# Optimization experiments

Measured on AMD Instinct MI355X. Metric: run time of the kernel, lower is better.

Reference implementation:

```python
import jax, jax.numpy as jnp
import numpy as np

B, N, D_FEAT = 16, 4096, 64
NPOINT, NSAMPLE = 1024, 32
MLP = [64, 64, 128]
IN_CH = 3 + D_FEAT
EPS = 1e-5  # BatchNorm eps (torch default)


def _fps(xyz, npoint):
    # Farthest point sampling; sequential scan over npoint steps (matches torch loop).
    b, n, _ = xyz.shape
    def step(carry, _):
        distance, farthest = carry  # (B,N) running min dist, (B,) current centroid idx
        centroid = jnp.take_along_axis(xyz, farthest[:, None, None], axis=1)  # (B,1,3)
        d = jnp.sum((xyz - centroid) ** 2, -1)  # (B,N)
        distance = jnp.minimum(distance, d)
        nxt = jnp.argmax(distance, -1).astype(jnp.int32)
        return (distance, nxt), farthest
    init = (jnp.full((b, n), jnp.inf, dtype=xyz.dtype),
            jnp.full((b,), n // 2, dtype=jnp.int32))
    _, centroids = jax.lax.scan(step, init, None, length=npoint)
    return centroids.T  # (B, npoint)


def _gather(pts, idx):
    # pts: (B,N,C); idx: (B,...) int -> (B,...,C)
    return jax.vmap(lambda p, i: p[i])(pts, idx)


def setup_inputs() -> dict:
    key = jax.random.key(0)
    ks = jax.random.split(key, 16)
    inp = {
        'xyz': jax.random.normal(ks[0], (B, N, 3), jnp.float32),
        'points': jax.random.normal(ks[1], (B, N, D_FEAT), jnp.float32),
    }
    last = IN_CH
    for li, oc in enumerate(MLP):
        inp[f'W{li}'] = jax.random.normal(ks[2 + li], (oc, last), jnp.float32) * (1.0 / np.sqrt(last))
        inp[f'b{li}'] = jnp.zeros((oc,), jnp.float32)
        inp[f'g{li}'] = jnp.ones((oc,), jnp.float32)
        inp[f'be{li}'] = jnp.zeros((oc,), jnp.float32)
        last = oc
    C = MLP[-1]; R = C // 8
    inp['aW1'] = jax.random.normal(ks[10], (R, C), jnp.float32) * (1.0 / np.sqrt(C))
    inp['aW2'] = jax.random.normal(ks[11], (C, R), jnp.float32) * (1.0 / np.sqrt(R))
    return inp


def reference(xyz, points, W0, b0, g0, be0, W1, b1, g1, be1, W2, b2, g2, be2, aW1, aW2):
    fps_idx = _fps(xyz, NPOINT)                 # (B,S) int32
    new_xyz = _gather(xyz, fps_idx)             # (B,S,3)
    # squared distances (B,S,N) via matmul expansion (as torch square_distance)
    d = (-2.0 * jnp.einsum('bsc,bnc->bsn', new_xyz, xyz)
         + jnp.sum(new_xyz ** 2, -1)[..., None]
         + jnp.sum(xyz ** 2, -1)[:, None, :])
    _, idx = jax.lax.top_k(-d, NSAMPLE)         # (B,S,k) nearest neighbors
    grouped_xyz = _gather(xyz, idx)             # (B,S,k,3)
    rel = grouped_xyz - new_xyz[:, :, None, :]  # relative coords
    feat = _gather(points, idx)                 # (B,S,k,D)
    g = jnp.concatenate([rel, feat], axis=-1)   # (B,S,k,3+D) channels-last
    # 1x1 conv MLP + BatchNorm (training-mode batch stats) + ReLU
    for (W, b, ga, be) in ((W0, b0, g0, be0), (W1, b1, g1, be1), (W2, b2, g2, be2)):
        g = jnp.einsum('bskc,oc->bsko', g, W) + b
        mu = g.mean(axis=(0, 1, 2))
        var = g.var(axis=(0, 1, 2))
        g = ga * (g - mu) * jax.lax.rsqrt(var + EPS) + be
        g = jax.nn.relu(g)
    new_points = g.max(axis=2)                  # max over nsample -> (B,S,C)
    # channel attention on (B,C,S) == reductions over S here
    avg = new_points.mean(axis=1)               # (B,C)
    mx = new_points.max(axis=1)                 # (B,C)
    def fc(v):
        return jnp.einsum('cr,br->bc', aW2, jax.nn.relu(jnp.einsum('rc,bc->br', aW1, v)))
    scale = jax.nn.sigmoid(fc(avg) + fc(mx))    # (B,C)
    new_points = new_points * scale[:, None, :]
    return new_xyz, new_points, fps_idx
```

## Files before the change

### kernel.cpp

```cpp
#include <hip/hip_runtime.h>
#include <hip/hip_bf16.h>

#define BB 16
#define NN 4096
#define SS 1024
#define KS 32
#define DF 64
#define INC 67
#define C1 64
#define C2 64
#define C3 128
#define ROWS (BB*SS*KS)
#define EPSBN 1e-5f
#define F_INF (__builtin_inff())

typedef __bf16 bf16;
typedef __bf16 bfrag __attribute__((ext_vector_type(8)));
typedef float  ffrag __attribute__((ext_vector_type(4)));
typedef float  f2    __attribute__((ext_vector_type(2)));
typedef unsigned long long u64;

#define OUT_NXYZ 0
#define OUT_NP   49152
#define OUT_FPS  2146304

#define OFF_FPS   0u
#define OFF_NXYZ  65536u
#define OFF_IDX   262144u
#define OFF_STATS 2359296u
#define OFF_ASUM  2555904u
#define OFF_AMAX  2621440u
#define OFF_BNC   2686976u
#define OFF_SCALE 2690048u
#define OFF_NP0   2698240u
#define OFF_YMAX  11086848u
#define OFF_H1    19475456u
#define OFF_H2    86584320u
#define ZERO_BYTES (196608u + 65536u + 65536u)

#define DPP_MAX_STEP(k, ctrl, rmask, bc) { \
  int _lo = __builtin_amdgcn_update_dpp(0, (int)(unsigned)(k), (ctrl), (rmask), 0xf, (bc)); \
  int _hi = __builtin_amdgcn_update_dpp(0, (int)((k)>>32),     (ctrl), (rmask), 0xf, (bc)); \
  u64 _k2 = ((u64)(unsigned)_hi << 32) | (unsigned)_lo; \
  if (_k2 > (k)) (k) = _k2; }

#define DPP_FMAX_STEP(v, ctrl, rmask, bc) { \
  int _t = __builtin_amdgcn_update_dpp(0, __float_as_int(v), (ctrl), (rmask), 0xf, (bc)); \
  (v) = fmaxf((v), __uint_as_float((unsigned)_t)); }

__device__ __forceinline__ u64 dpp_wavemax64(u64 k){
  DPP_MAX_STEP(k, 0x111, 0xf, true)
  DPP_MAX_STEP(k, 0x112, 0xf, true)
  DPP_MAX_STEP(k, 0x114, 0xf, true)
  DPP_MAX_STEP(k, 0x118, 0xf, true)
  DPP_MAX_STEP(k, 0x142, 0xa, false)
  DPP_MAX_STEP(k, 0x143, 0xc, false)
  return k;
}

__device__ __forceinline__ u64 readlane64(u64 k, int lane){
  unsigned lo = (unsigned)__builtin_amdgcn_readlane((int)(unsigned)k, lane);
  unsigned hi = (unsigned)__builtin_amdgcn_readlane((int)(k >> 32),   lane);
  return ((u64)hi << 32) | lo;
}

__device__ __forceinline__ u64 umax64(u64 a, u64 b){ return a > b ? a : b; }

__global__ __launch_bounds__(256) void fps_kernel(const float* __restrict__ xyz,
                                                  int* __restrict__ fps_i,
                                                  float* __restrict__ nxyz_ws,
                                                  float* __restrict__ out)
{
  #pragma clang fp contract(off)
  __shared__ __align__(16) float4 lc[NN];
  __shared__ int lfps[SS];
  __shared__ __align__(16) u64 slotk[2][4];
  int b = blockIdx.x, t = threadIdx.x;
  const float* xb = xyz + (size_t)b*NN*3;
  for (int p = t; p < NN; p += 256){
    lc[p] = make_float4(xb[p*3], xb[p*3+1], xb[p*3+2], 0.f);
  }
  __syncthreads();
  f2 px2[8], py2[8], pz2[8], pd2[8];
  int p0 = t*16;
  #pragma unroll
  for (int j=0;j<8;++j){
    float4 a = lc[p0+2*j], c = lc[p0+2*j+1];
    px2[j] = (f2){a.x, c.x}; py2[j] = (f2){a.y, c.y}; pz2[j] = (f2){a.z, c.z};
    pd2[j] = (f2){F_INF, F_INF};
  }
  float cx = lc[NN/2].x, cy = lc[NN/2].y, cz = lc[NN/2].z;
  if (t==0) lfps[0]=NN/2;
  int wv = t >> 6, lane = t & 63;
  for (int it=1; it<SS; ++it){
    f2 c2x = (f2){cx,cx}, c2y = (f2){cy,cy}, c2z = (f2){cz,cz};
    float bv=-1.f; int bi=p0;
    #pragma unroll
    for (int j=0;j<8;++j){
      f2 dx = px2[j]-c2x, dy = py2[j]-c2y, dz = pz2[j]-c2z;
      f2 d = (dx*dx + dy*dy) + dz*dz;
      f2 nd = (f2){fminf(pd2[j].x, d.x), fminf(pd2[j].y, d.y)};
      pd2[j]=nd;
      if (nd.x > bv){ bv=nd.x; bi=p0+2*j; }
      if (nd.y > bv){ bv=nd.y; bi=p0+2*j+1; }
    }
    float mv = bv;
    DPP_FMAX_STEP(mv, 0x111, 0xf, true)
    DPP_FMAX_STEP(mv, 0x112, 0xf, true)
    DPP_FMAX_STEP(mv, 0x114, 0xf, true)
    DPP_FMAX_STEP(mv, 0x118, 0xf, true)
    DPP_FMAX_STEP(mv, 0x142, 0xa, false)
    DPP_FMAX_STEP(mv, 0x143, 0xc, false)
    float wmax = __uint_as_float((unsigned)__builtin_amdgcn_readlane(__float_as_int(mv), 63));
    u64 em = __ballot(bv == wmax);
    int wl = (int)__builtin_ctzll(em);
    int wbi = __builtin_amdgcn_readlane(bi, wl);
    int p = it & 1;
    if (lane == 0)
      slotk[p][wv] = ((u64)__float_as_uint(wmax) << 32) | (unsigned)(~wbi);
    __syncthreads();
    ulonglong2 sA = *(const ulonglong2*)&slotk[p][0];
    ulonglong2 sB = *(const ulonglong2*)&slotk[p][2];
    u64 k = umax64(umax64(sA.x, sA.y), umax64(sB.x, sB.y));
    int i = ~(unsigned)k;
    float4 cc = lc[i];
    cx = cc.x; cy = cc.y; cz = cc.z;
    if (t==0) lfps[it]=i;
  }
  __syncthreads();
  for (int s=t; s<SS; s+=256){
    int i = lfps[s];
    fps_i[b*SS+s]=i;
    out[OUT_FPS + b*SS + s] = (float)i;
    float4 cc = lc[i];
    int o3 = (b*SS+s)*3;
    out[OUT_NXYZ+o3]=cc.x; out[OUT_NXYZ+o3+1]=cc.y; out[OUT_NXYZ+o3+2]=cc.z;
    nxyz_ws[o3]=cc.x; nxyz_ws[o3+1]=cc.y; nxyz_ws[o3+2]=cc.z;
  }
}

__global__ __launch_bounds__(64) void knn_kernel(const float* __restrict__ xyz,
                                                 const float* __restrict__ nxyz,
                                                 int* __restrict__ knn)
{
  __shared__ float ld[NN];
  int lane = threadIdx.x;
  int bs = blockIdx.x;
  int b = bs >> 10;
  const float* xb = xyz + (size_t)b*NN*3;
  float sx=nxyz[bs*3], sy=nxyz[bs*3+1], sz=nxyz[bs*3+2];
  float gv[8]; int gi[8];
  float lv = F_INF; int li = 0;
  #pragma unroll
  for (int g=0; g<8; ++g){
    float bgv = F_INF; int bgi = 0;
    #pragma unroll
    for (int jj=0; jj<8; ++jj){
      int p = (g*8+jj)*64 + lane;
      float dx=xb[p*3]-sx, dy=xb[p*3+1]-sy, dz=xb[p*3+2]-sz;
      float d = dx*dx+dy*dy+dz*dz;
      ld[p] = d;
      if (d < bgv){ bgv=d; bgi=p; }
    }
    gv[g]=bgv; gi[g]=bgi;
    if (bgv < lv){ lv=bgv; li=bgi; }
  }
  int kept = 0;
  for (int it=0; it<KS; ++it){
    u64 mk = ~(((u64)__float_as_uint(lv) << 32) | (unsigned)li);
    mk = dpp_wavemax64(mk);
    mk = readlane64(mk, 63);
    int i = (int)(unsigned)(~mk);
    if (lane==it) kept = i;
    if ((i & 63) == lane){
      int j = i >> 6;
      ld[i] = F_INF;
      int g = j >> 3;
      float bgv=F_INF; int bgi=0;
      for (int jj=0;jj<8;++jj){
        int p = (g*8+jj)*64 + lane;
        float d = ld[p];
        if (d<bgv){bgv=d;bgi=p;}
      }
      #pragma unroll
      for (int q=0;q<8;++q){ if (q==g){ gv[q]=bgv; gi[q]=bgi; } }
      lv=F_INF; li=0;
      #pragma unroll
      for (int q=0;q<8;++q){ if (gv[q]<lv){ lv=gv[q]; li=gi[q]; } }
    }
  }
  if (lane < KS) knn[bs*KS + lane] = kept;
}

__global__ __launch_bounds__(512) void conv1_kernel(const float* __restrict__ xyz,
                                                    const float* __restrict__ points,
                                                    const float* __restrict__ W0,
                                                    const float* __restrict__ b0,
                                                    const float* __restrict__ nxyz,
                                                    const int* __restrict__ knn,
                                                    bf16* __restrict__ h1,
                                                    float* __restrict__ stats)
{
  __shared__ __align__(16) bf16 As[128][104];
  __shared__ __align__(16) bf16 Bs[64][104];
  __shared__ float s1[C1], s2[C1];
  int t = threadIdx.x;
  int Rbase = blockIdx.x * 128;
  if (t < C1){ s1[t]=0.f; s2[t]=0.f; }
  if (t < 256){
    int o = t >> 2, q = t & 3;
    const float* wr = W0 + o*INC;
    for (int cc = q*24; cc < q*24+24; ++cc){
      float w;
      if (cc < 64) w = wr[3+cc];
      else if (cc < 67) w = wr[cc-64];
      else w = 0.f;
      Bs[o][cc] = (bf16)w;
    }
  }
  {
    int r = t >> 2, q = t & 3;
    int R = Rbase + r;
    int bs = R >> 5;
    int bIdx = bs >> 10;
    int nI = knn[R];
    const float* pr = points + ((size_t)(bIdx*NN + nI))*DF + q*16;
    float4 f0 = *(const float4*)(pr);
    float4 f1 = *(const float4*)(pr+4);
    float4 f2v = *(const float4*)(pr+8);
    float4 f3 = *(const float4*)(pr+12);
    bf16* ap = &As[r][q*16];
    ap[0]=(bf16)f0.x; ap[1]=(bf16)f0.y; ap[2]=(bf16)f0.z; ap[3]=(bf16)f0.w;
    ap[4]=(bf16)f1.x; ap[5]=(bf16)f1.y; ap[6]=(bf16)f1.z; ap[7]=(bf16)f1.w;
    ap[8]=(bf16)f2v.x; ap[9]=(bf16)f2v.y; ap[10]=(bf16)f2v.z; ap[11]=(bf16)f2v.w;
    ap[12]=(bf16)f3.x; ap[13]=(bf16)f3.y; ap[14]=(bf16)f3.z; ap[15]=(bf16)f3.w;
    if (q==0){
      const float* xr = xyz + ((size_t)(bIdx*NN + nI))*3;
      const float* nr = nxyz + bs*3;
      As[r][64]=(bf16)(xr[0]-nr[0]);
      As[r][65]=(bf16)(xr[1]-nr[1]);
      As[r][66]=(bf16)(xr[2]-nr[2]);
      for (int cc=67; cc<96; ++cc) As[r][cc]=(bf16)0.f;
    }
  }
  __syncthreads();
  int wv = t >> 6, lane = t & 63;
  int row16 = wv * 16;
  int arow = lane & 15, kgrp = lane >> 4;
  ffrag acc[4] = {};
  #pragma unroll
  for (int kc = 0; kc < 3; ++kc){
    bfrag af = *(const bfrag*)&As[row16 + arow][kc*32 + kgrp*8];
    #pragma unroll
    for (int nt = 0; nt < 4; ++nt){
      bfrag bfv = *(const bfrag*)&Bs[nt*16 + arow][kc*32 + kgrp*8];
      acc[nt] = __builtin_amdgcn_mfma_f32_16x16x32_bf16(af, bfv, acc[nt], 0,0,0);
    }
  }
  #pragma unroll
  for (int nt=0; nt<4; ++nt){
    int c = nt*16 + arow;
    float bias = b0[c];
    float ls1=0.f, ls2=0.f;
    #pragma unroll
    for (int r=0;r<4;++r){
      float y = acc[nt][r] + bias;
      int grow = Rbase + row16 + kgrp*4 + r;
      h1[(size_t)grow*C1 + c] = (bf16)y;
      ls1 += y; ls2 += y*y;
    }
    ls1 += __shfl_xor(ls1, 16); ls1 += __shfl_xor(ls1, 32);
    ls2 += __shfl_xor(ls2, 16); ls2 += __shfl_xor(ls2, 32);
    if (kgrp==0){ atomicAdd(&s1[c], ls1); atomicAdd(&s2[c], ls2); }
  }
  __syncthreads();
  if (t < C1){
    float* gp = stats + (blockIdx.x & 63)*256;
    atomicAdd(&gp[t], s1[t]);
    atomicAdd(&gp[128 + t], s2[t]);
  }
}

__global__ __launch_bounds__(512) void conv2_kernel(const bf16* __restrict__ h1,
                                                    const float* __restrict__ W1,
                                                    const float* __restrict__ b1,
                                                    const float* __restrict__ stats0,
                                                    const float* __restrict__ g0,
                                                    const float* __restrict__ be0,
                                                    bf16* __restrict__ h2,
                                                    float* __restrict__ stats)
{
  __shared__ __align__(16) bf16 As[128][72];
  __shared__ __align__(16) bf16 Bs[64][72];
  __shared__ float s1[C2], s2[C2];
  __shared__ float sbA[C2], sbB[C2];
  int t = threadIdx.x;
  int Rbase = blockIdx.x * 128;
  if (t < C2){ s1[t]=0.f; s2[t]=0.f; }
  if (t < C2){
    float a1=0.f, a2=0.f;
    for (int q=0;q<64;++q){ a1 += stats0[q*256+t]; a2 += stats0[q*256+128+t]; }
    float inv = 1.f/(float)ROWS;
    float mu = a1*inv; float var = a2*inv - mu*mu;
    float a = g0[t]*rsqrtf(var + EPSBN);
    sbA[t] = a; sbB[t] = be0[t] - mu*a;
  }
  if (t < 256){
    int o = t >> 2, q = t & 3;
    const float* wr = W1 + o*64 + q*16;
    bf16* bp = &Bs[o][q*16];
    #pragma unroll
    for (int v=0; v<4; ++v){
      float4 f = *(const float4*)(wr + v*4);
      bp[v*4+0]=(bf16)f.x; bp[v*4+1]=(bf16)f.y; bp[v*4+2]=(bf16)f.z; bp[v*4+3]=(bf16)f.w;
    }
  }
  __syncthreads();
  {
    int r = t >> 2, q = t & 3;
    int R = Rbase + r;
    const bf16* hr = h1 + (size_t)R*64 + q*16;
    bfrag h0 = *(const bfrag*)hr;
    bfrag h1v = *(const bfrag*)(hr+8);
    #pragma unroll
    for (int j=0;j<8;++j){
      int c=q*16+j;
      As[r][c] = (bf16)fmaxf(fmaf(sbA[c], (float)h0[j], sbB[c]), 0.f);
    }
    #pragma unroll
    for (int j=0;j<8;++j){
      int c=q*16+8+j;
      As[r][c] = (bf16)fmaxf(fmaf(sbA[c], (float)h1v[j], sbB[c]), 0.f);
    }
  }
  __syncthreads();
  int wv = t >> 6, lane = t & 63;
  int row16 = wv * 16;
  int arow = lane & 15, kgrp = lane >> 4;
  ffrag acc[4] = {};
  #pragma unroll
  for (int kc = 0; kc < 2; ++kc){
    bfrag af = *(const bfrag*)&As[row16 + arow][kc*32 + kgrp*8];
    #pragma unroll
    for (int nt = 0; nt < 4; ++nt){
      bfrag bfv = *(const bfrag*)&Bs[nt*16 + arow][kc*32 + kgrp*8];
      acc[nt] = __builtin_amdgcn_mfma_f32_16x16x32_bf16(af, bfv, acc[nt], 0,0,0);
    }
  }
  #pragma unroll
  for (int nt=0; nt<4; ++nt){
    int c = nt*16 + arow;
    float bias = b1[c];
    float ls1=0.f, ls2=0.f;
    #pragma unroll
    for (int r=0;r<4;++r){
      float y = acc[nt][r] + bias;
      int grow = Rbase + row16 + kgrp*4 + r;
      h2[(size_t)grow*C2 + c] = (bf16)y;
      ls1 += y; ls2 += y*y;
    }
    ls1 += __shfl_xor(ls1, 16); ls1 += __shfl_xor(ls1, 32);
    ls2 += __shfl_xor(ls2, 16); ls2 += __shfl_xor(ls2, 32);
    if (kgrp==0){ atomicAdd(&s1[c], ls1); atomicAdd(&s2[c], ls2); }
  }
  __syncthreads();
  if (t < C2){
    float* gp = stats + (blockIdx.x & 63)*256;
    atomicAdd(&gp[t], s1[t]);
    atomicAdd(&gp[128 + t], s2[t]);
  }
}

__global__ __launch_bounds__(512) void conv3_kernel(const bf16* __restrict__ h2,
                                                    const float* __restrict__ W2,
                                                    const float* __restrict__ b2,
                                                    const float* __restrict__ stats1,
                                                    const float* __restrict__ g1,
                                                    const float* __restrict__ be1,
                                                    float* __restrict__ ymax,
                                                    float* __restrict__ stats)
{
  __shared__ __align__(16) bf16 As[128][72];
  __shared__ __align__(16) bf16 Bs[128][72];
  __shared__ float s1[C3], s2[C3];
  __shared__ float wmax[8][C3];
  __shared__ float sbA[C2], sbB[C2];
  int t = threadIdx.x;
  int Rbase = blockIdx.x * 128;
  if (t < C3){ s1[t]=0.f; s2[t]=0.f; }
  if (t < C2){
    float a1=0.f, a2=0.f;
    for (int q=0;q<64;++q){ a1 += stats1[q*256+t]; a2 += stats1[q*256+128+t]; }
    float inv = 1.f/(float)ROWS;
    float mu = a1*inv; float var = a2*inv - mu*mu;
    float a = g1[t]*rsqrtf(var + EPSBN);
    sbA[t] = a; sbB[t] = be1[t] - mu*a;
  }
  if (t < 256){
    int o = t >> 1, q = t & 1;
    const float* wr = W2 + o*64 + q*32;
    bf16* bp = &Bs[o][q*32];
    #pragma unroll
    for (int v=0; v<8; ++v){
      float4 f = *(const float4*)(wr + v*4);
      bp[v*4+0]=(bf16)f.x; bp[v*4+1]=(bf16)f.y; bp[v*4+2]=(bf16)f.z; bp[v*4+3]=(bf16)f.w;
    }
  }
  __syncthreads();
  {
    int r = t >> 2, q = t & 3;
    int R = Rbase + r;
    const bf16* hr = h2 + (size_t)R*64 + q*16;
    bfrag h0 = *(const bfrag*)hr;
    bfrag h1v = *(const bfrag*)(hr+8);
    #pragma unroll
    for (int j=0;j<8;++j){
      int c=q*16+j;
      As[r][c] = (bf16)fmaxf(fmaf(sbA[c], (float)h0[j], sbB[c]), 0.f);
    }
    #pragma unroll
    for (int j=0;j<8;++j){
      int c=q*16+8+j;
      As[r][c] = (bf16)fmaxf(fmaf(sbA[c], (float)h1v[j], sbB[c]), 0.f);
    }
  }
  __syncthreads();
  int wv = t >> 6, lane = t & 63;
  int row16 = wv * 16;
  int arow = lane & 15, kgrp = lane >> 4;
  ffrag acc[8] = {};
  #pragma unroll
  for (int kc = 0; kc < 2; ++kc){
    bfrag af = *(const bfrag*)&As[row16 + arow][kc*32 + kgrp*8];
    #pragma unroll
    for (int nt = 0; nt < 8; ++nt){
      bfrag bfv = *(const bfrag*)&Bs[nt*16 + arow][kc*32 + kgrp*8];
      acc[nt] = __builtin_amdgcn_mfma_f32_16x16x32_bf16(af, bfv, acc[nt], 0,0,0);
    }
  }
  #pragma unroll
  for (int nt=0; nt<8; ++nt){
    int c = nt*16 + arow;
    float bias = b2[c];
    float ls1=0.f, ls2=0.f, mm=-F_INF;
    #pragma unroll
    for (int r=0;r<4;++r){
      float y = acc[nt][r] + bias;
      ls1 += y; ls2 += y*y; mm = fmaxf(mm, y);
    }
    ls1 += __shfl_xor(ls1, 16); ls1 += __shfl_xor(ls1, 32);
    ls2 += __shfl_xor(ls2, 16); ls2 += __shfl_xor(ls2, 32);
    mm = fmaxf(mm, __shfl_xor(mm, 16)); mm = fmaxf(mm, __shfl_xor(mm, 32));
    if (kgrp==0){ atomicAdd(&s1[c], ls1); atomicAdd(&s2[c], ls2); wmax[wv][c]=mm; }
  }
  __syncthreads();
  {
    int grp = t >> 7;
    int c = t & 127;
    float m = fmaxf(wmax[grp*2][c], wmax[grp*2+1][c]);
    ymax[(size_t)(blockIdx.x*4 + grp)*C3 + c] = m;
  }
  if (t < C3){
    float* gp = stats + (blockIdx.x & 63)*256;
    atomicAdd(&gp[t], s1[t]);
    atomicAdd(&gp[128 + t], s2[t]);
  }
}

__global__ __launch_bounds__(256) void attreduce_kernel(const float* __restrict__ ymax,
                                                        const float* __restrict__ stats2,
                                                        const float* __restrict__ g2,
                                                        const float* __restrict__ be2,
                                                        float* __restrict__ np0,
                                                        float* __restrict__ asum,
                                                        unsigned* __restrict__ amax)
{
  __shared__ float rs[256], rm[256];
  __shared__ float sbA[C3], sbB[C3];
  int t = threadIdx.x;
  if (t < C3){
    float a1=0.f, a2=0.f;
    for (int q=0;q<64;++q){ a1 += stats2[q*256+t]; a2 += stats2[q*256+128+t]; }
    float inv = 1.f/(float)ROWS;
    float mu = a1*inv; float var = a2*inv - mu*mu;
    float a = g2[t]*rsqrtf(var + EPSBN);
    sbA[t] = a; sbB[t] = be2[t] - mu*a;
  }
  __syncthreads();
  int b = blockIdx.x >> 3, sg = blockIdx.x & 7;
  int c = t & 127, h = t >> 7;
  float a = sbA[c], bb = sbB[c];
  size_t base = ((size_t)(b*1024 + sg*128 + h*64))*128 + c;
  float s = 0.f, m = 0.f;
  #pragma unroll 4
  for (int j=0;j<64;++j){
    float v = fmaxf(fmaf(a, ymax[base + (size_t)j*128], bb), 0.f);
    np0[base + (size_t)j*128] = v;
    s += v; m = fmaxf(m, v);
  }
  rs[t]=s; rm[t]=m;
  __syncthreads();
  if (t < 128){
    float s2 = rs[t] + rs[t+128];
    float m2 = fmaxf(rm[t], rm[t+128]);
    atomicAdd(&asum[b*128+t], s2);
    atomicMax(&amax[b*128+t], __float_as_uint(m2));
  }
}

__global__ __launch_bounds__(256) void attn_kernel(const float* __restrict__ asum,
                                                   const unsigned* __restrict__ amax,
                                                   const float* __restrict__ aW1,
                                                   const float* __restrict__ aW2,
                                                   float* __restrict__ scale)
{
  __shared__ float avg[16][128], mx[16][128], hA[16][16], hM[16][16];
  int t = threadIdx.x;
  for (int i=t; i<2048; i+=256){
    int b=i>>7, c=i&127;
    avg[b][c]=asum[i]*(1.f/1024.f); mx[b][c]=__uint_as_float(amax[i]);
  }
  __syncthreads();
  {
    int b=t>>4, r=t&15;
    float sa=0.f, sm=0.f;
    for (int c=0;c<128;++c){ float w=aW1[r*128+c]; sa+=w*avg[b][c]; sm+=w*mx[b][c]; }
    hA[b][r]=fmaxf(sa,0.f); hM[b][r]=fmaxf(sm,0.f);
  }
  __syncthreads();
  for (int i=t;i<2048;i+=256){
    int b=i>>7,c=i&127;
    float o=0.f;
    for (int r=0;r<16;++r){ o += aW2[c*16+r]*(hA[b][r]+hM[b][r]); }
    scale[i] = 1.f/(1.f+expf(-o));
  }
}

__global__ __launch_bounds__(256) void finout_kernel(const float* __restrict__ np0,
                                                     const float* __restrict__ scale,
                                                     float* __restrict__ out)
{
  int i = blockIdx.x*256 + threadIdx.x;
  int c = i & 127; int b = i >> 17;
  out[OUT_NP + i] = np0[i] * scale[b*128+c];
}

extern "C" void kernel_launch(void* const* d_in, const int* in_sizes, int n_in,
                              void* d_out, int out_size, void* d_ws, size_t ws_size,
                              hipStream_t stream)
{
  const float* xyz    = (const float*)d_in[0];
  const float* points = (const float*)d_in[1];
  const float* W0 = (const float*)d_in[2];
  const float* b0 = (const float*)d_in[3];
  const float* g0 = (const float*)d_in[4];
  const float* be0= (const float*)d_in[5];
  const float* W1 = (const float*)d_in[6];
  const float* b1 = (const float*)d_in[7];
  const float* g1 = (const float*)d_in[8];
  const float* be1= (const float*)d_in[9];
  const float* W2 = (const float*)d_in[10];
  const float* b2 = (const float*)d_in[11];
  const float* g2 = (const float*)d_in[12];
  const float* be2= (const float*)d_in[13];
  const float* aW1= (const float*)d_in[14];
  const float* aW2= (const float*)d_in[15];
  float* out = (float*)d_out;
  char* ws = (char*)d_ws;

  int*      fpsI  = (int*)(ws + OFF_FPS);
  float*    nxyz  = (float*)(ws + OFF_NXYZ);
  int*      knnI  = (int*)(ws + OFF_IDX);
  float*    stats = (float*)(ws + OFF_STATS);
  float*    asum  = (float*)(ws + OFF_ASUM);
  unsigned* amax  = (unsigned*)(ws + OFF_AMAX);
  float*    scl   = (float*)(ws + OFF_SCALE);
  float*    np0   = (float*)(ws + OFF_NP0);
  float*    ymax  = (float*)(ws + OFF_YMAX);
  bf16*     h1    = (bf16*)(ws + OFF_H1);
  bf16*     h2    = (bf16*)(ws + OFF_H2);

  hipMemsetAsync(ws + OFF_STATS, 0, ZERO_BYTES, stream);
  fps_kernel<<<BB, 256, 0, stream>>>(xyz, fpsI, nxyz, out);
  knn_kernel<<<BB*SS, 64, 0, stream>>>(xyz, nxyz, knnI);
  conv1_kernel<<<ROWS/128, 512, 0, stream>>>(xyz, points, W0, b0, nxyz, knnI, h1, stats);
  conv2_kernel<<<ROWS/128, 512, 0, stream>>>(h1, W1, b1, stats, g0, be0, h2, stats + 64*256);
  conv3_kernel<<<ROWS/128, 512, 0, stream>>>(h2, W2, b2, stats + 64*256, g1, be1, ymax, stats + 2*64*256);
  attreduce_kernel<<<BB*8, 256, 0, stream>>>(ymax, stats + 2*64*256, g2, be2, np0, asum, amax);
  attn_kernel<<<1, 256, 0, stream>>>(asum, amax, aW1, aW2, scl);
  finout_kernel<<<(BB*SS*C3)/256, 256, 0, stream>>>(np0, scl, out);
}
```

Measured before the change: 1.024 ms.

## Pad xyz to float4 for kNN, drop np0 buffer, widen attreduce grid

FPS now also writes a float4-padded copy of xyz to the workspace, so kNN can do one vector load per point instead of three strided scalar loads. The attreduce kernel no longer writes the normalized np0 tensor. It stores the BN scale and shift so finout can recompute the BN+ReLU from ymax, which removes an 8 MB write and read. The attreduce grid is widened from 128 to 512 blocks to add parallelism. The cost is an extra 1 MB write in FPS and more atomics in attreduce.

```diff
diff --git a/kernel.cpp b/kernel.cpp
--- a/kernel.cpp
+++ b/kernel.cpp
@@ -32,7 +32,7 @@
 #define OFF_AMAX  2621440u
 #define OFF_BNC   2686976u
 #define OFF_SCALE 2690048u
-#define OFF_NP0   2698240u
+#define OFF_XYZ4  2698240u
 #define OFF_YMAX  11086848u
 #define OFF_H1    19475456u
 #define OFF_H2    86584320u
@@ -69,6 +69,7 @@
 __global__ __launch_bounds__(256) void fps_kernel(const float* __restrict__ xyz,
                                                   int* __restrict__ fps_i,
                                                   float* __restrict__ nxyz_ws,
+                                                  float4* __restrict__ xyz4,
                                                   float* __restrict__ out)
 {
   #pragma clang fp contract(off)
@@ -81,6 +82,7 @@
     lc[p] = make_float4(xb[p*3], xb[p*3+1], xb[p*3+2], 0.f);
   }
   __syncthreads();
+  for (int p = t; p < NN; p += 256) xyz4[(size_t)b*NN + p] = lc[p];
   f2 px2[8], py2[8], pz2[8], pd2[8];
   int p0 = t*16;
   #pragma unroll
@@ -139,7 +141,7 @@
   }
 }
 
-__global__ __launch_bounds__(64) void knn_kernel(const float* __restrict__ xyz,
+__global__ __launch_bounds__(64) void knn_kernel(const float4* __restrict__ xyz4,
                                                  const float* __restrict__ nxyz,
                                                  int* __restrict__ knn)
 {
@@ -147,7 +149,7 @@
   int lane = threadIdx.x;
   int bs = blockIdx.x;
   int b = bs >> 10;
-  const float* xb = xyz + (size_t)b*NN*3;
+  const float4* xb4 = xyz4 + (size_t)b*NN;
   float sx=nxyz[bs*3], sy=nxyz[bs*3+1], sz=nxyz[bs*3+2];
   float gv[8]; int gi[8];
   float lv = F_INF; int li = 0;
@@ -157,7 +159,8 @@
     #pragma unroll
     for (int jj=0; jj<8; ++jj){
       int p = (g*8+jj)*64 + lane;
-      float dx=xb[p*3]-sx, dy=xb[p*3+1]-sy, dz=xb[p*3+2]-sz;
+      float4 P = xb4[p];
+      float dx=P.x-sx, dy=P.y-sy, dz=P.z-sz;
       float d = dx*dx+dy*dy+dz*dz;
       ld[p] = d;
       if (d < bgv){ bgv=d; bgi=p; }
@@ -471,7 +474,7 @@
                                                         const float* __restrict__ stats2,
                                                         const float* __restrict__ g2,
                                                         const float* __restrict__ be2,
-                                                        float* __restrict__ np0,
+                                                        float* __restrict__ bnc,
                                                         float* __restrict__ asum,
                                                         unsigned* __restrict__ amax)
 {
@@ -485,17 +488,17 @@
     float mu = a1*inv; float var = a2*inv - mu*mu;
     float a = g2[t]*rsqrtf(var + EPSBN);
     sbA[t] = a; sbB[t] = be2[t] - mu*a;
-  }
-  __syncthreads();
-  int b = blockIdx.x >> 3, sg = blockIdx.x & 7;
+    if (blockIdx.x == 0){ bnc[t] = a; bnc[128+t] = sbB[t]; }
+  }
+  __syncthreads();
+  int b = blockIdx.x >> 5, sg = blockIdx.x & 31;
   int c = t & 127, h = t >> 7;
   float a = sbA[c], bb = sbB[c];
-  size_t base = ((size_t)(b*1024 + sg*128 + h*64))*128 + c;
+  size_t base = ((size_t)(b*1024 + sg*32 + h*16))*128 + c;
   float s = 0.f, m = 0.f;
   #pragma unroll 4
-  for (int j=0;j<64;++j){
+  for (int j=0;j<16;++j){
     float v = fmaxf(fmaf(a, ymax[base + (size_t)j*128], bb), 0.f);
-    np0[base + (size_t)j*128] = v;
     s += v; m = fmaxf(m, v);
   }
   rs[t]=s; rm[t]=m;
@@ -536,13 +539,15 @@
   }
 }
 
-__global__ __launch_bounds__(256) void finout_kernel(const float* __restrict__ np0,
+__global__ __launch_bounds__(256) void finout_kernel(const float* __restrict__ ymax,
+                                                     const float* __restrict__ bnc,
                                                      const float* __restrict__ scale,
                                                      float* __restrict__ out)
 {
   int i = blockIdx.x*256 + threadIdx.x;
   int c = i & 127; int b = i >> 17;
-  out[OUT_NP + i] = np0[i] * scale[b*128+c];
+  float v = fmaxf(fmaf(bnc[c], ymax[i], bnc[128+c]), 0.f);
+  out[OUT_NP + i] = v * scale[b*128+c];
 }
 
 extern "C" void kernel_launch(void* const* d_in, const int* in_sizes, int n_in,
@@ -574,19 +579,20 @@
   float*    stats = (float*)(ws + OFF_STATS);
   float*    asum  = (float*)(ws + OFF_ASUM);
   unsigned* amax  = (unsigned*)(ws + OFF_AMAX);
+  float*    bnc   = (float*)(ws + OFF_BNC);
   float*    scl   = (float*)(ws + OFF_SCALE);
-  float*    np0   = (float*)(ws + OFF_NP0);
+  float4*   xyz4  = (float4*)(ws + OFF_XYZ4);
   float*    ymax  = (float*)(ws + OFF_YMAX);
   bf16*     h1    = (bf16*)(ws + OFF_H1);
   bf16*     h2    = (bf16*)(ws + OFF_H2);
 
   hipMemsetAsync(ws + OFF_STATS, 0, ZERO_BYTES, stream);
-  fps_kernel<<<BB, 256, 0, stream>>>(xyz, fpsI, nxyz, out);
-  knn_kernel<<<BB*SS, 64, 0, stream>>>(xyz, nxyz, knnI);
+  fps_kernel<<<BB, 256, 0, stream>>>(xyz, fpsI, nxyz, xyz4, out);
+  knn_kernel<<<BB*SS, 64, 0, stream>>>(xyz4, nxyz, knnI);
   conv1_kernel<<<ROWS/128, 512, 0, stream>>>(xyz, points, W0, b0, nxyz, knnI, h1, stats);
   conv2_kernel<<<ROWS/128, 512, 0, stream>>>(h1, W1, b1, stats, g0, be0, h2, stats + 64*256);
   conv3_kernel<<<ROWS/128, 512, 0, stream>>>(h2, W2, b2, stats + 64*256, g1, be1, ymax, stats + 2*64*256);
-  attreduce_kernel<<<BB*8, 256, 0, stream>>>(ymax, stats + 2*64*256, g2, be2, np0, asum, amax);
+  attreduce_kernel<<<512, 256, 0, stream>>>(ymax, stats + 2*64*256, g2, be2, bnc, asum, amax);
   attn_kernel<<<1, 256, 0, stream>>>(asum, amax, aW1, aW2, scl);
-  finout_kernel<<<(BB*SS*C3)/256, 256, 0, stream>>>(np0, scl, out);
-}
+  finout_kernel<<<(BB*SS*C3)/256, 256, 0, stream>>>(ymax, bnc, scl, out);
+}
```

New measurement: 1.026 ms. No clear change (+0.3%).
